# Kernel optimization log

Hardware: AMD Instinct MI355X
Metric: run time of the kernel (lower is better)

The kernel has to match this reference:

```python
import jax, jax.numpy as jnp
import numpy as np

B, N, D = 1, 4096, 512
H, HD = 8, 64
NBINS = 512
CAND = 64
SCALE = 1.0 / np.sqrt(HD)
MAX_NORM = 1.0 - 1e-5
TWO_PI = 2.0 * np.pi


def _project(x):
    # Poincare-ball style projection: clip L2 norm of each point to MAX_NORM.
    n = jnp.sqrt(jnp.sum(x * x, axis=-1, keepdims=True))
    s = jnp.minimum(1.0, MAX_NORM / jnp.maximum(n, 1e-12))
    return x * s


def _bins(x):
    # Deterministic geometric binning (DavisCache stand-in): quantize the
    # angle of the first two coordinates into NBINS bins.
    ang = jnp.arctan2(x[..., 1], x[..., 0])  # (-pi, pi]
    b = jnp.floor((ang / TWO_PI + 0.5) * NBINS)
    return jnp.clip(b, 0, NBINS - 1).astype(jnp.int32)


def setup_inputs() -> dict:
    key0 = jax.random.key(0)
    ks = jax.random.split(key0, 12)
    w = 0.02  # typical init scale for projection weights
    return {
        "query": jax.random.normal(ks[0], (B, N, D), dtype=jnp.float32),
        "key": jax.random.normal(ks[1], (B, N, D), dtype=jnp.float32),
        "value": jax.random.normal(ks[2], (B, N, D), dtype=jnp.float32),
        "Wq": jax.random.normal(ks[3], (D, D), dtype=jnp.float32) * w,
        "bq": jnp.zeros((D,), dtype=jnp.float32),
        "Wk": jax.random.normal(ks[4], (D, D), dtype=jnp.float32) * w,
        "bk": jnp.zeros((D,), dtype=jnp.float32),
        "Wv": jax.random.normal(ks[5], (D, D), dtype=jnp.float32) * w,
        "bv": jnp.zeros((D,), dtype=jnp.float32),
        "Wo": jax.random.normal(ks[6], (D, D), dtype=jnp.float32) * w,
        "bo": jnp.zeros((D,), dtype=jnp.float32),
    }


def reference(query, key, value, Wq, bq, Wk, bk, Wv, bv, Wo, bo):
    Bq, Nq, Dm = query.shape
    Nk = key.shape[1]
    # projections + split heads -> (B, H, N, HD)
    q = (query @ Wq.T + bq).reshape(Bq, Nq, H, HD).transpose(0, 2, 1, 3)
    k = (key @ Wk.T + bk).reshape(Bq, Nk, H, HD).transpose(0, 2, 1, 3)
    v = (value @ Wv.T + bv).reshape(Bq, Nk, H, HD).transpose(0, 2, 1, 3)
    q = _project(q)
    k = _project(k)

    # geometric binning; candidate keys for a query are those whose bin is
    # within radius 1 of the query's bin (neighboring_bins, radius=1).
    qb = _bins(q)  # (B, H, Nq) int32
    kb = _bins(k)  # (B, H, Nk) int32
    mask = jnp.abs(qb[..., :, None] - kb[..., None, :]) <= 1  # (B,H,Nq,Nk)
    # fallback: if a query has no candidates, attend over all keys
    any_valid = jnp.any(mask, axis=-1, keepdims=True)
    eff = jnp.where(any_valid, mask, True)
    # keep only the first CAND candidates per query (by key index)
    rank = jnp.cumsum(eff.astype(jnp.int32), axis=-1) - 1
    sel = eff & (rank < CAND)

    scores = jnp.einsum("bhqd,bhkd->bhqk", q, k) * SCALE
    scores = jnp.where(sel, scores, -jnp.inf)
    attn = jax.nn.softmax(scores, axis=-1)  # dropout p=0.0 (eval mode)
    out = jnp.einsum("bhqk,bhkd->bhqd", attn, v)

    out = out.transpose(0, 2, 1, 3).reshape(Bq, Nq, Dm)
    return out @ Wo.T + bo
```

## Files before the change

kernel.cpp:

```cpp
#include <hip/hip_runtime.h>
#include <math.h>

typedef unsigned short u16;
typedef __attribute__((ext_vector_type(8))) short v8bf;
typedef __attribute__((ext_vector_type(4))) float f32x4;

#define N_TOK 4096
#define DMODEL 512
#define NHEAD 8
#define HDIM 64
#define CANDN 64
#define NBINS 512
#define BINCAP 64
#define QCAP 128
#define ATT_SCALE 0.125f
#define MAX_NORM_F 0.99999f

__device__ __forceinline__ float bf2f(u16 u) {
  union { unsigned int i; float f; } v; v.i = ((unsigned int)u) << 16; return v.f;
}
__device__ __forceinline__ u16 f2bf(float f) {
  union { float f; unsigned int i; } v; v.f = f;
  unsigned int x = v.i;
  return (u16)((x + 0x7fffu + ((x >> 16) & 1u)) >> 16);
}
__device__ __forceinline__ uint4 load_pack8(const float* __restrict__ p) {
  const float4 x0 = *(const float4*)p;
  const float4 x1 = *(const float4*)(p + 4);
  union { u16 h[8]; uint4 u; } r;
  r.h[0] = f2bf(x0.x); r.h[1] = f2bf(x0.y); r.h[2] = f2bf(x0.z); r.h[3] = f2bf(x0.w);
  r.h[4] = f2bf(x1.x); r.h[5] = f2bf(x1.y); r.h[6] = f2bf(x1.z); r.h[7] = f2bf(x1.w);
  return r.u;
}

__global__ __launch_bounds__(256) void prep_kernel(
    const float* __restrict__ query, const float* __restrict__ key_,
    const float* __restrict__ value,
    const float* __restrict__ Wq, const float* __restrict__ Wk,
    const float* __restrict__ Wv, const float* __restrict__ Wo,
    u16* __restrict__ qx, u16* __restrict__ kx, u16* __restrict__ vx,
    u16* __restrict__ wqx, u16* __restrict__ wkx, u16* __restrict__ wvx,
    u16* __restrict__ wox,
    int* __restrict__ qb, int* __restrict__ kb, unsigned char* __restrict__ flags,
    int* __restrict__ khist)
{
  __shared__ float xs[16 * 516];
  const int blk = blockIdx.x;
  const int tid = threadIdx.x;

  if (blk >= 512) {
    const int base = ((blk - 512) << 8) + tid;
    for (int u = base; u < 919552; u += 262144) {
      if (u < 786432) {
        const int third = u >> 18;
        const int off = (u & 262143) << 3;
        const float* src = (third == 0) ? query : (third == 1) ? key_ : value;
        u16* dst = (third == 0) ? qx : (third == 1) ? kx : vx;
        *(uint4*)(dst + off) = load_pack8(src + off);
      } else if (u < 917504) {
        const int r2 = u - 786432;
        const int w = r2 >> 15;
        const int off = (r2 & 32767) << 3;
        const float* src = (w == 0) ? Wq : (w == 1) ? Wk : (w == 2) ? Wv : Wo;
        u16* dst = (w == 0) ? wqx : (w == 1) ? wkx : (w == 2) ? wvx : wox;
        *(uint4*)(dst + off) = load_pack8(src + off);
      } else {
        int4 z4; z4.x = 0; z4.y = 0; z4.z = 0; z4.w = 0;
        ((int4*)khist)[u - 917504] = z4;
      }
    }
    return;
  }

  const int isk  = blk >> 8;
  const int tile = blk & 255;
  const float* X = isk ? key_ : query;
  const float* W = isk ? Wk : Wq;

#pragma unroll
  for (int i = 0; i < 8; ++i) {
    const int flat = i * 1024 + tid * 4;
    const int row = flat >> 9, col = flat & 511;
    *(float4*)&xs[row * 516 + col] = *(const float4*)(X + (tile * 16 + row) * DMODEL + col);
  }
  __syncthreads();

  const int n_local = tid >> 4;
  const int pair = tid & 15;
  const int h = pair >> 1, coord = pair & 1;
  const float* wrow = W + ((h << 6) + coord) * DMODEL;
  const float* xrow = &xs[n_local * 516];

  double c0 = 0.0, c1 = 0.0, c2 = 0.0, c3 = 0.0;
  for (int k = 0; k < DMODEL; k += 4) {
    const float4 xv = *(const float4*)(xrow + k);
    const float4 wv = *(const float4*)(wrow + k);
    c0 = fma((double)xv.x, (double)wv.x, c0);
    c1 = fma((double)xv.y, (double)wv.y, c1);
    c2 = fma((double)xv.z, (double)wv.z, c2);
    c3 = fma((double)xv.w, (double)wv.w, c3);
  }
  const double a = (c0 + c1) + (c2 + c3);
  const double other = __shfl_xor(a, 1);
  if (coord == 0) {
    const double a0 = a, a1 = other;
    const int n = tile * 16 + n_local;
    double ang = atan2(a1, a0);
    double t = (ang / 6.283185307179586 + 0.5) * 512.0;
    int b = (int)floor(t);
    b = b < 0 ? 0 : (b > 511 ? 511 : b);
    (isk ? kb : qb)[(h << 12) + n] = b;

    const double r = sqrt(a0 * a0 + a1 * a1);
    const double dist = fabs(t - nearbyint(t));
    const double margin = fmin(0.45, 3.3e-4 / fmax(r, 1e-30) + 5e-5);
    flags[(isk << 15) | (h << 12) | n] = (dist < margin) ? 1 : 0;
  }
}

__device__ float fdlibm_atanf(float x) {
#pragma clang fp contract(off)
  const float atanhi[4] = {4.6364760399e-01f, 7.8539812565e-01f,
                           9.8279368877e-01f, 1.5707962513e+00f};
  const float atanlo[4] = {5.0121582440e-09f, 3.7748947079e-08f,
                           3.4473217170e-08f, 7.5497894159e-08f};
  const float aT[5] = {3.3333328366e-01f, -1.9999158382e-01f, 1.4253635705e-01f,
                       -1.0648017377e-01f, 6.1687607318e-02f};
  unsigned ix = __float_as_uint(x);
  const unsigned sign = ix >> 31;
  ix &= 0x7fffffffu;
  int id;
  float z, w, s1, s2;
  if (ix >= 0x4c800000u) {
    z = atanhi[3] + 0x1p-120f;
    return sign ? -z : z;
  }
  if (ix < 0x3ee00000u) {
    if (ix < 0x39800000u) return x;
    id = -1;
  } else {
    x = fabsf(x);
    if (ix < 0x3f980000u) {
      if (ix < 0x3f300000u) { id = 0; x = (2.0f * x - 1.0f) / (2.0f + x); }
      else                  { id = 1; x = (x - 1.0f) / (x + 1.0f); }
    } else {
      if (ix < 0x401c0000u) { id = 2; x = (x - 1.5f) / (1.0f + 1.5f * x); }
      else                  { id = 3; x = -1.0f / x; }
    }
  }
  z = x * x;
  w = z * z;
  s1 = z * (aT[0] + w * (aT[2] + w * aT[4]));
  s2 = w * (aT[1] + w * aT[3]);
  if (id < 0) return x - x * (s1 + s2);
  z = atanhi[id] - ((x * (s1 + s2) - atanlo[id]) - x);
  return sign ? -z : z;
}

__device__ float fdlibm_atan2f(float y, float x) {
#pragma clang fp contract(off)
  const float pi = 3.1415927410e+00f, pi_lo = -8.7422776573e-08f;
  const unsigned hx = __float_as_uint(x), hy = __float_as_uint(y);
  if (hx == 0x3f800000u) return fdlibm_atanf(y);
  const unsigned m = ((hy >> 31) & 1u) | ((hx >> 30) & 2u);
  const unsigned ix = hx & 0x7fffffffu, iy = hy & 0x7fffffffu;
  if (iy == 0u) {
    switch (m) { case 0: case 1: return y; case 2: return pi; default: return -pi; }
  }
  if (ix == 0u) return (m & 1u) ? -1.57079637050628662f : 1.57079637050628662f;
  float z;
  if (ix + (26u << 23) < iy) {
    z = 1.57079637050628662f;
    return (m & 1u) ? -z : z;
  }
  if ((m & 2u) && iy + (26u << 23) < ix) z = 0.0f;
  else z = fdlibm_atanf(fabsf(y / x));
  switch (m) {
    case 0: return z;
    case 1: return -z;
    case 2: return pi - (z - pi_lo);
    default: return (z - pi_lo) - pi;
  }
}

__global__ __launch_bounds__(256) void binfix_kernel(
    const float* __restrict__ query, const float* __restrict__ key_,
    const float* __restrict__ Wq, const float* __restrict__ Wk,
    const unsigned char* __restrict__ flags,
    int* __restrict__ qb, int* __restrict__ kb)
{
  __shared__ int wle[64];
  __shared__ int wlc;

  const int tid = threadIdx.x;
  const int slice = blockIdx.x;

  if (tid == 0) wlc = 0;
  __syncthreads();
  if (tid < 128) {
    const int flat = (slice << 7) + tid;
    if (flags[flat]) {
      const int p = atomicAdd(&wlc, 1);
      if (p < 64) wle[p] = flat;
    }
  }
  __syncthreads();
  int nw = wlc; if (nw > 64) nw = 64;
  const int w = tid >> 6, d = tid & 63;
  for (int e = w; e < nw; e += 4) {
    const int flat = wle[e];
    const int n = flat & 4095;
    const int h = (flat >> 12) & 7;
    const int isk = flat >> 15;
    const float* xr = (isk ? key_ : query) + n * DMODEL;
    const float* wr = (isk ? Wk : Wq) + ((h << 6) + d) * DMODEL;
    float acc = 0.0f;
    for (int k = 0; k < DMODEL; k += 16) {
      const float4 xa = *(const float4*)(xr + k);
      const float4 xb = *(const float4*)(xr + k + 4);
      const float4 xc = *(const float4*)(xr + k + 8);
      const float4 xd = *(const float4*)(xr + k + 12);
      const float4 wa = *(const float4*)(wr + k);
      const float4 wb = *(const float4*)(wr + k + 4);
      const float4 wc = *(const float4*)(wr + k + 8);
      const float4 wd = *(const float4*)(wr + k + 12);
      acc = __fmaf_rn(xa.x, wa.x, acc); acc = __fmaf_rn(xa.y, wa.y, acc);
      acc = __fmaf_rn(xa.z, wa.z, acc); acc = __fmaf_rn(xa.w, wa.w, acc);
      acc = __fmaf_rn(xb.x, wb.x, acc); acc = __fmaf_rn(xb.y, wb.y, acc);
      acc = __fmaf_rn(xb.z, wb.z, acc); acc = __fmaf_rn(xb.w, wb.w, acc);
      acc = __fmaf_rn(xc.x, wc.x, acc); acc = __fmaf_rn(xc.y, wc.y, acc);
      acc = __fmaf_rn(xc.z, wc.z, acc); acc = __fmaf_rn(xc.w, wc.w, acc);
      acc = __fmaf_rn(xd.x, wd.x, acc); acc = __fmaf_rn(xd.y, wd.y, acc);
      acc = __fmaf_rn(xd.z, wd.z, acc); acc = __fmaf_rn(xd.w, wd.w, acc);
    }
    {
#pragma clang fp contract(off)
      const float sq = acc * acc;
      float rr[8];
#pragma unroll
      for (int j = 0; j < 8; ++j) rr[j] = __shfl(sq, j);
      for (int i = 8; i < 64; i += 8) {
#pragma unroll
        for (int j = 0; j < 8; ++j) rr[j] += __shfl(sq, i + j);
      }
      const float ss = ((rr[0] + rr[1]) + (rr[2] + rr[3])) +
                       ((rr[4] + rr[5]) + (rr[6] + rr[7]));
      const float nrm = __fsqrt_rn(ss);
      const float s = fminf(1.0f, 0.99999f / fmaxf(nrm, 1e-12f));
      const float c0 = __shfl(acc, 0) * s;
      const float c1 = __shfl(acc, 1) * s;
      const float cr = (float)atan2((double)c1, (double)c0);
      const float fd = fdlibm_atan2f(c1, c0);
      const float tol = fmaxf(fabsf(cr) * 6e-7f, 1e-30f);
      const float ang = (fabsf(fd - cr) <= tol) ? fd : cr;
      const float t = ((ang / 6.2831854820251465f) + 0.5f) * 512.0f;
      int b = (int)floorf(t);
      b = b < 0 ? 0 : (b > 511 ? 511 : b);
      if (d == 0) (isk ? kb : qb)[(h << 12) + n] = b;
    }
  }
}

__global__ __launch_bounds__(256) void gemm_qkv_kernel(
    const u16* __restrict__ qx, const u16* __restrict__ kx, const u16* __restrict__ vx,
    const u16* __restrict__ wqx, const u16* __restrict__ wkx, const u16* __restrict__ wvx,
    const float* __restrict__ bq, const float* __restrict__ bk, const float* __restrict__ bv,
    u16* __restrict__ Qb, u16* __restrict__ Kb, u16* __restrict__ Vb)
{
  __shared__ u16 As[2][128 * 40];
  __shared__ u16 Ws[2][128 * 40];

  const int blk = blockIdx.x;
  const int tid = threadIdx.x;

  const int z = blk >> 7;
  const int rem = blk & 127;
  const int bm = (rem & 31) * 128;
  const int bn = (rem >> 5) * 128;

  const u16* A    = (z == 0) ? qx : (z == 1) ? kx : vx;
  const u16* W    = (z == 0) ? wqx : (z == 1) ? wkx : wvx;
  const float* bias = (z == 0) ? bq : (z == 1) ? bk : bv;
  u16* O          = (z == 0) ? Qb : (z == 1) ? Kb : Vb;

  const int lane = tid & 63;
  const int wave = tid >> 6;
  const int row4 = tid >> 2;
  const int seg  = tid & 3;
  const int wm = (wave & 1) * 64;
  const int wn = (wave >> 1) * 64;
  const int l15 = lane & 15;
  const int quad = lane >> 4;

  f32x4 acc[4][4] = {};

  uint4 a0 = *(const uint4*)(A + (bm + row4) * DMODEL + seg * 8);
  uint4 a1 = *(const uint4*)(A + (bm + row4 + 64) * DMODEL + seg * 8);
  uint4 w0 = *(const uint4*)(W + (bn + row4) * DMODEL + seg * 8);
  uint4 w1 = *(const uint4*)(W + (bn + row4 + 64) * DMODEL + seg * 8);

  for (int kt = 0; kt < DMODEL; kt += 32) {
    const int p = (kt >> 5) & 1;
    *(uint4*)&As[p][row4 * 40 + seg * 8] = a0;
    *(uint4*)&As[p][(row4 + 64) * 40 + seg * 8] = a1;
    *(uint4*)&Ws[p][row4 * 40 + seg * 8] = w0;
    *(uint4*)&Ws[p][(row4 + 64) * 40 + seg * 8] = w1;
    __syncthreads();
    if (kt + 32 < DMODEL) {
      a0 = *(const uint4*)(A + (bm + row4) * DMODEL + kt + 32 + seg * 8);
      a1 = *(const uint4*)(A + (bm + row4 + 64) * DMODEL + kt + 32 + seg * 8);
      w0 = *(const uint4*)(W + (bn + row4) * DMODEL + kt + 32 + seg * 8);
      w1 = *(const uint4*)(W + (bn + row4 + 64) * DMODEL + kt + 32 + seg * 8);
    }
    v8bf af[4], bfr[4];
#pragma unroll
    for (int i = 0; i < 4; ++i)
      af[i] = *(const v8bf*)&As[p][(wm + i * 16 + l15) * 40 + quad * 8];
#pragma unroll
    for (int j = 0; j < 4; ++j)
      bfr[j] = *(const v8bf*)&Ws[p][(wn + j * 16 + l15) * 40 + quad * 8];
#pragma unroll
    for (int i = 0; i < 4; ++i)
#pragma unroll
      for (int j = 0; j < 4; ++j)
        acc[i][j] = __builtin_amdgcn_mfma_f32_16x16x32_bf16(af[i], bfr[j], acc[i][j], 0, 0, 0);
  }

  float bval[4];
#pragma unroll
  for (int j = 0; j < 4; ++j) bval[j] = bias[bn + wn + j * 16 + l15];
  const int h = (bn + wn) >> 6;

#pragma unroll
  for (int i = 0; i < 4; ++i) {
#pragma unroll
    for (int r = 0; r < 4; ++r) {
      const int row = bm + wm + i * 16 + quad * 4 + r;
      float v0 = acc[i][0][r] + bval[0];
      float v1 = acc[i][1][r] + bval[1];
      float v2 = acc[i][2][r] + bval[2];
      float v3 = acc[i][3][r] + bval[3];
      if (z != 2) {
        float ss = v0 * v0 + v1 * v1 + v2 * v2 + v3 * v3;
#pragma unroll
        for (int o = 1; o < 16; o <<= 1) ss += __shfl_xor(ss, o);
        const float s = fminf(1.0f, MAX_NORM_F / fmaxf(sqrtf(ss), 1e-12f));
        v0 *= s; v1 *= s; v2 *= s; v3 *= s;
      }
      const int base = (((h << 12) + row) << 6) + l15;
      O[base +  0] = f2bf(v0); O[base + 16] = f2bf(v1);
      O[base + 32] = f2bf(v2); O[base + 48] = f2bf(v3);
    }
  }
}

__global__ __launch_bounds__(256) void bin_hist_kernel(
    const int* __restrict__ kb, const int* __restrict__ qb,
    int* __restrict__ khist, u16* __restrict__ blist,
    int* __restrict__ qhist, u16* __restrict__ qlist)
{
  const int h = blockIdx.x;
  const int type = blockIdx.y;
  const int* src = type ? qb : kb;
  int* hist = type ? qhist : khist;
  u16* list = type ? qlist : blist;
  const int cap = type ? QCAP : BINCAP;

  const int i = blockIdx.z * 256 + threadIdx.x;
  const int b = src[(h << 12) + i];
  const int pos = atomicAdd(&hist[(h << 9) + b], 1);
  if (pos < cap) list[((h << 9) + b) * cap + pos] = (u16)i;
}

__global__ __launch_bounds__(64) void attn_bin_kernel(
    const u16* __restrict__ Qb, const u16* __restrict__ Kb,
    const u16* __restrict__ Vb, const int* __restrict__ qhist,
    const u16* __restrict__ qlist, const int* __restrict__ khist,
    const u16* __restrict__ blist, u16* __restrict__ aout)
{
  __shared__ u16 kf[4 * 2 * 4 * 16 * 8];
  __shared__ u16 vf[4 * 2 * 4 * 16 * 8];
  __shared__ u16 pf[16 * 72];
  __shared__ u16 s_cand[64];
  __shared__ int s_qg[16];

  const int hb = blockIdx.x;
  const int h = hb >> 9;
  const int b = hb & 511;
  int qcnt = qhist[hb];
  if (qcnt > QCAP) qcnt = QCAP;
  if (qcnt == 0) return;

  const int lane = threadIdx.x;
  const int l15 = lane & 15;
  const int quad = lane >> 4;

  int v0 = 0xFFFF, v1 = 0xFFFF, v2 = 0xFFFF;
  int c0 = 0, c1 = 0, c2 = 0;
  if (b > 0) {
    c0 = khist[(h << 9) + b - 1];
    if (c0 > BINCAP) c0 = BINCAP;
    if (lane < c0) v0 = (int)blist[(((h << 9) + b - 1) << 6) + lane];
  }
  {
    c1 = khist[(h << 9) + b];
    if (c1 > BINCAP) c1 = BINCAP;
    if (lane < c1) v1 = (int)blist[(((h << 9) + b) << 6) + lane];
  }
  if (b < NBINS - 1) {
    c2 = khist[(h << 9) + b + 1];
    if (c2 > BINCAP) c2 = BINCAP;
    if (lane < c2) v2 = (int)blist[(((h << 9) + b + 1) << 6) + lane];
  }

  int r0 = 0, r1 = 0, r2 = 0;
#pragma unroll 8
  for (int j = 0; j < 64; ++j) {
    const int w0 = __shfl(v0, j);
    const int w1 = __shfl(v1, j);
    const int w2 = __shfl(v2, j);
    r0 += (w0 < v0) + (w1 < v0) + (w2 < v0);
    r1 += (w0 < v1) + (w1 < v1) + (w2 < v1);
    r2 += (w0 < v2) + (w1 < v2) + (w2 < v2);
  }
  const int tot = c0 + c1 + c2;
  const int ccnt = tot < CANDN ? tot : CANDN;
  const int ccnt_eff = (tot == 0) ? 64 : ccnt;
  if (tot == 0) {
    s_cand[lane] = (u16)lane;
  } else {
    if (v0 != 0xFFFF && r0 < CANDN) s_cand[r0] = (u16)v0;
    if (v1 != 0xFFFF && r1 < CANDN) s_cand[r1] = (u16)v1;
    if (v2 != 0xFFFF && r2 < CANDN) s_cand[r2] = (u16)v2;
  }
  __syncthreads();
  if (tot > 0 && lane >= ccnt) s_cand[lane] = s_cand[0];
  __syncthreads();

  {
    const int r = lane >> 3, s = lane & 7;
    const int ks = s >> 2, qd = s & 3;
#pragma unroll
    for (int it = 0; it < 8; ++it) {
      const int key = it * 8 + r;
      const int c = s_cand[key];
      const uint4 kv = *(const uint4*)(Kb + ((h << 18) | (c << 6)) + s * 8);
      const int idx = ((((key >> 4) * 2 + ks) * 4 + qd) * 16 + (key & 15)) * 8;
      *(uint4*)&kf[idx] = kv;
    }
  }
  {
    const int r = lane >> 3, s = lane & 7;
    const int nt = s >> 1, d0 = (s & 1) * 8;
#pragma unroll
    for (int it = 0; it < 8; ++it) {
      const int key = it * 8 + r;
      const int c = s_cand[key];
      union { u16 hh[8]; uint4 u; } vv;
      vv.u = *(const uint4*)(Vb + ((h << 18) | (c << 6)) + s * 8);
      const int kstep = key >> 5, qd = (key >> 3) & 3, j = key & 7;
#pragma unroll
      for (int m = 0; m < 8; ++m)
        vf[(((nt * 2 + kstep) * 4 + qd) * 16 + d0 + m) * 8 + j] = vv.hh[m];
    }
  }
  __syncthreads();

  v8bf akf[4][2], bvf[4][2];
#pragma unroll
  for (int t = 0; t < 4; ++t)
#pragma unroll
    for (int ks = 0; ks < 2; ++ks) {
      akf[t][ks] = *(const v8bf*)&kf[(((t * 2 + ks) * 4 + quad) * 16 + l15) * 8];
      bvf[t][ks] = *(const v8bf*)&vf[(((t * 2 + ks) * 4 + quad) * 16 + l15) * 8];
    }

  const int nchunk = (qcnt + 15) >> 4;
  for (int ci = 0; ci < nchunk; ++ci) {
    const int base = ci << 4;
    const int qcn = min(16, qcnt - base);
    __syncthreads();
    if (lane < 16) {
      int idx = base + lane;
      if (idx > qcnt - 1) idx = qcnt - 1;
      s_qg[lane] = (int)qlist[(hb << 7) + idx];
    }
    __syncthreads();

    const u16* qrow = Qb + ((h << 18) | (s_qg[l15] << 6));
    v8bf bq[2];
#pragma unroll
    for (int ks = 0; ks < 2; ++ks)
      bq[ks] = *(const v8bf*)(qrow + ks * 32 + quad * 8);

    float sc[16];
    __builtin_amdgcn_s_setprio(1);
#pragma unroll
    for (int t = 0; t < 4; ++t) {
      f32x4 sa = {0.f, 0.f, 0.f, 0.f};
      sa = __builtin_amdgcn_mfma_f32_16x16x32_bf16(akf[t][0], bq[0], sa, 0, 0, 0);
      sa = __builtin_amdgcn_mfma_f32_16x16x32_bf16(akf[t][1], bq[1], sa, 0, 0, 0);
#pragma unroll
      for (int r = 0; r < 4; ++r) {
        const int key = t * 16 + quad * 4 + r;
        sc[t * 4 + r] = (key < ccnt_eff) ? sa[r] * ATT_SCALE : -INFINITY;
      }
    }
    __builtin_amdgcn_s_setprio(0);
    float mx = sc[0];
#pragma unroll
    for (int i = 1; i < 16; ++i) mx = fmaxf(mx, sc[i]);
    mx = fmaxf(mx, __shfl_xor(mx, 16));
    mx = fmaxf(mx, __shfl_xor(mx, 32));
    float sum = 0.0f;
    float pe[16];
#pragma unroll
    for (int i = 0; i < 16; ++i) { pe[i] = __expf(sc[i] - mx); sum += pe[i]; }
    sum += __shfl_xor(sum, 16);
    sum += __shfl_xor(sum, 32);
    const float inv = 1.0f / sum;

    __syncthreads();
#pragma unroll
    for (int t = 0; t < 4; ++t)
#pragma unroll
      for (int r = 0; r < 4; ++r)
        pf[l15 * 72 + t * 16 + quad * 4 + r] = f2bf(pe[t * 4 + r] * inv);
    __syncthreads();

    v8bf ap[2];
#pragma unroll
    for (int ks = 0; ks < 2; ++ks)
      ap[ks] = *(const v8bf*)&pf[l15 * 72 + ks * 32 + quad * 8];

    __builtin_amdgcn_s_setprio(1);
#pragma unroll
    for (int nt = 0; nt < 4; ++nt) {
      f32x4 o = {0.f, 0.f, 0.f, 0.f};
      o = __builtin_amdgcn_mfma_f32_16x16x32_bf16(ap[0], bvf[nt][0], o, 0, 0, 0);
      o = __builtin_amdgcn_mfma_f32_16x16x32_bf16(ap[1], bvf[nt][1], o, 0, 0, 0);
#pragma unroll
      for (int r = 0; r < 4; ++r) {
        const int row = quad * 4 + r;
        if (row < qcn)
          aout[s_qg[row] * DMODEL + (h << 6) + nt * 16 + l15] = f2bf(o[r]);
      }
    }
    __builtin_amdgcn_s_setprio(0);
  }
}

__global__ __launch_bounds__(256) void gemm_out_kernel(
    const u16* __restrict__ A, const u16* __restrict__ W,
    const float* __restrict__ bias, float* __restrict__ O)
{
  __shared__ u16 As[2][64 * 40];
  __shared__ u16 Ws[2][128 * 40];

  const int tid  = threadIdx.x;
  const int lane = tid & 63;
  const int wave = tid >> 6;
  const int row4 = tid >> 2;
  const int seg  = tid & 3;

  const int bm = blockIdx.x * 64;
  const int bn = blockIdx.y * 128;
  const int wm = (wave & 1) * 32;
  const int wn = (wave >> 1) * 64;
  const int l15 = lane & 15;
  const int quad = lane >> 4;

  f32x4 acc[2][4] = {};

  uint4 a0 = *(const uint4*)(A + (bm + row4) * DMODEL + seg * 8);
  uint4 w0 = *(const uint4*)(W + (bn + row4) * DMODEL + seg * 8);
  uint4 w1 = *(const uint4*)(W + (bn + row4 + 64) * DMODEL + seg * 8);

  for (int kt = 0; kt < DMODEL; kt += 32) {
    const int p = (kt >> 5) & 1;
    *(uint4*)&As[p][row4 * 40 + seg * 8] = a0;
    *(uint4*)&Ws[p][row4 * 40 + seg * 8] = w0;
    *(uint4*)&Ws[p][(row4 + 64) * 40 + seg * 8] = w1;
    __syncthreads();
    if (kt + 32 < DMODEL) {
      a0 = *(const uint4*)(A + (bm + row4) * DMODEL + kt + 32 + seg * 8);
      w0 = *(const uint4*)(W + (bn + row4) * DMODEL + kt + 32 + seg * 8);
      w1 = *(const uint4*)(W + (bn + row4 + 64) * DMODEL + kt + 32 + seg * 8);
    }
    v8bf af[2], bfr[4];
#pragma unroll
    for (int i = 0; i < 2; ++i)
      af[i] = *(const v8bf*)&As[p][(wm + i * 16 + l15) * 40 + quad * 8];
#pragma unroll
    for (int j = 0; j < 4; ++j)
      bfr[j] = *(const v8bf*)&Ws[p][(wn + j * 16 + l15) * 40 + quad * 8];
#pragma unroll
    for (int i = 0; i < 2; ++i)
#pragma unroll
      for (int j = 0; j < 4; ++j)
        acc[i][j] = __builtin_amdgcn_mfma_f32_16x16x32_bf16(af[i], bfr[j], acc[i][j], 0, 0, 0);
  }

#pragma unroll
  for (int j = 0; j < 4; ++j) {
    const int cg = bn + wn + j * 16 + l15;
    const float bval = bias[cg];
#pragma unroll
    for (int i = 0; i < 2; ++i) {
      const int rbase = bm + wm + i * 16 + quad * 4;
#pragma unroll
      for (int r = 0; r < 4; ++r)
        O[(rbase + r) * DMODEL + cg] = acc[i][j][r] + bval;
    }
  }
}

extern "C" void kernel_launch(void* const* d_in, const int* in_sizes, int n_in,
                              void* d_out, int out_size, void* d_ws, size_t ws_size,
                              hipStream_t stream) {
  const float* query = (const float*)d_in[0];
  const float* key_  = (const float*)d_in[1];
  const float* value = (const float*)d_in[2];
  const float* Wq = (const float*)d_in[3];
  const float* bq = (const float*)d_in[4];
  const float* Wk = (const float*)d_in[5];
  const float* bk = (const float*)d_in[6];
  const float* Wv = (const float*)d_in[7];
  const float* bv = (const float*)d_in[8];
  const float* Wo = (const float*)d_in[9];
  const float* bo = (const float*)d_in[10];

  char* ws = (char*)d_ws;
  u16* qx    = (u16*)(ws);
  u16* kx    = (u16*)(ws + 4194304);
  u16* vx    = (u16*)(ws + 8388608);
  u16* wqx   = (u16*)(ws + 12582912);
  u16* wkx   = (u16*)(ws + 13107200);
  u16* wvx   = (u16*)(ws + 13631488);
  u16* wox   = (u16*)(ws + 14155776);
  u16* Qb    = (u16*)(ws + 14680064);
  u16* Kb    = (u16*)(ws + 18874368);
  u16* Vb    = (u16*)(ws + 23068672);
  u16* aout  = (u16*)(ws + 27262976);
  int* qb    = (int*)(ws + 31457280);
  int* kb    = (int*)(ws + 31588352);
  unsigned char* flags = (unsigned char*)(ws + 31719424);
  int* khist = (int*)(ws + 31784960);
  int* qhist = (int*)(ws + 31801344);
  u16* blist = (u16*)(ws + 31817728);
  u16* qlist = (u16*)(ws + 32342016);

  prep_kernel<<<1536, 256, 0, stream>>>(
      query, key_, value, Wq, Wk, Wv, Wo,
      qx, kx, vx, wqx, wkx, wvx, wox, qb, kb, flags, khist);
  binfix_kernel<<<512, 256, 0, stream>>>(
      query, key_, Wq, Wk, flags, qb, kb);
  gemm_qkv_kernel<<<384, 256, 0, stream>>>(
      qx, kx, vx, wqx, wkx, wvx, bq, bk, bv, Qb, Kb, Vb);
  bin_hist_kernel<<<dim3(8, 2, 16), 256, 0, stream>>>(
      kb, qb, khist, blist, qhist, qlist);
  attn_bin_kernel<<<4096, 64, 0, stream>>>(
      Qb, Kb, Vb, qhist, qlist, khist, blist, aout);
  gemm_out_kernel<<<dim3(64, 4), 256, 0, stream>>>(aout, wox, bo, (float*)d_out);
}
```

Measured before the change: 200.3 us.

## Fuse fp32-to-bf16 activation conversion into QKV GEMM and shrink GEMM tiles

The separate pass that converted query/key/value to bf16 in the prep kernel is removed. The QKV GEMM now reads fp32 activations directly and packs them to bf16 while staging into shared memory, which avoids writing and re-reading about 12 MB of intermediates. The QKV GEMM M-tile drops from 128 to 64 rows (768 blocks), and the output GEMM tile becomes 64x64 (512 blocks), giving more blocks for occupancy. The cost is twice the fp32 activation bytes per load inside the GEMM, redundant conversion of A across N-tiles, and less data reuse per block.

```diff
diff --git a/kernel.cpp b/kernel.cpp
--- a/kernel.cpp
+++ b/kernel.cpp
@@ -32,13 +32,17 @@
   r.h[4] = f2bf(x1.x); r.h[5] = f2bf(x1.y); r.h[6] = f2bf(x1.z); r.h[7] = f2bf(x1.w);
   return r.u;
 }
+__device__ __forceinline__ uint4 pack8v(const float4 x0, const float4 x1) {
+  union { u16 h[8]; uint4 u; } r;
+  r.h[0] = f2bf(x0.x); r.h[1] = f2bf(x0.y); r.h[2] = f2bf(x0.z); r.h[3] = f2bf(x0.w);
+  r.h[4] = f2bf(x1.x); r.h[5] = f2bf(x1.y); r.h[6] = f2bf(x1.z); r.h[7] = f2bf(x1.w);
+  return r.u;
+}
 
 __global__ __launch_bounds__(256) void prep_kernel(
     const float* __restrict__ query, const float* __restrict__ key_,
-    const float* __restrict__ value,
     const float* __restrict__ Wq, const float* __restrict__ Wk,
     const float* __restrict__ Wv, const float* __restrict__ Wo,
-    u16* __restrict__ qx, u16* __restrict__ kx, u16* __restrict__ vx,
     u16* __restrict__ wqx, u16* __restrict__ wkx, u16* __restrict__ wvx,
     u16* __restrict__ wox,
     int* __restrict__ qb, int* __restrict__ kb, unsigned char* __restrict__ flags,
@@ -49,25 +53,16 @@
   const int tid = threadIdx.x;
 
   if (blk >= 512) {
-    const int base = ((blk - 512) << 8) + tid;
-    for (int u = base; u < 919552; u += 262144) {
-      if (u < 786432) {
-        const int third = u >> 18;
-        const int off = (u & 262143) << 3;
-        const float* src = (third == 0) ? query : (third == 1) ? key_ : value;
-        u16* dst = (third == 0) ? qx : (third == 1) ? kx : vx;
-        *(uint4*)(dst + off) = load_pack8(src + off);
-      } else if (u < 917504) {
-        const int r2 = u - 786432;
-        const int w = r2 >> 15;
-        const int off = (r2 & 32767) << 3;
-        const float* src = (w == 0) ? Wq : (w == 1) ? Wk : (w == 2) ? Wv : Wo;
-        u16* dst = (w == 0) ? wqx : (w == 1) ? wkx : (w == 2) ? wvx : wox;
-        *(uint4*)(dst + off) = load_pack8(src + off);
-      } else {
-        int4 z4; z4.x = 0; z4.y = 0; z4.z = 0; z4.w = 0;
-        ((int4*)khist)[u - 917504] = z4;
-      }
+    const int u = ((blk - 512) << 8) + tid;
+    if (u < 131072) {
+      const int w = u >> 15;
+      const int off = (u & 32767) << 3;
+      const float* src = (w == 0) ? Wq : (w == 1) ? Wk : (w == 2) ? Wv : Wo;
+      u16* dst = (w == 0) ? wqx : (w == 1) ? wkx : (w == 2) ? wvx : wox;
+      *(uint4*)(dst + off) = load_pack8(src + off);
+    } else if (u < 133120) {
+      int4 z4; z4.x = 0; z4.y = 0; z4.z = 0; z4.w = 0;
+      ((int4*)khist)[u - 131072] = z4;
     }
     return;
   }
@@ -262,65 +257,65 @@
 }
 
 __global__ __launch_bounds__(256) void gemm_qkv_kernel(
-    const u16* __restrict__ qx, const u16* __restrict__ kx, const u16* __restrict__ vx,
+    const float* __restrict__ query, const float* __restrict__ key_,
+    const float* __restrict__ value,
     const u16* __restrict__ wqx, const u16* __restrict__ wkx, const u16* __restrict__ wvx,
     const float* __restrict__ bq, const float* __restrict__ bk, const float* __restrict__ bv,
     u16* __restrict__ Qb, u16* __restrict__ Kb, u16* __restrict__ Vb)
 {
-  __shared__ u16 As[2][128 * 40];
+  __shared__ u16 As[2][64 * 40];
   __shared__ u16 Ws[2][128 * 40];
 
   const int blk = blockIdx.x;
   const int tid = threadIdx.x;
 
-  const int z = blk >> 7;
-  const int rem = blk & 127;
-  const int bm = (rem & 31) * 128;
-  const int bn = (rem >> 5) * 128;
-
-  const u16* A    = (z == 0) ? qx : (z == 1) ? kx : vx;
+  const int z = blk >> 8;
+  const int rem = blk & 255;
+  const int bm = (rem & 63) * 64;
+  const int bn = (rem >> 6) * 128;
+
+  const float* X  = (z == 0) ? query : (z == 1) ? key_ : value;
   const u16* W    = (z == 0) ? wqx : (z == 1) ? wkx : wvx;
   const float* bias = (z == 0) ? bq : (z == 1) ? bk : bv;
   u16* O          = (z == 0) ? Qb : (z == 1) ? Kb : Vb;
 
   const int lane = tid & 63;
   const int wave = tid >> 6;
-  const int row4 = tid >> 2;
-  const int seg  = tid & 3;
-  const int wm = (wave & 1) * 64;
+  const int ra  = tid >> 2;
+  const int oa  = (tid & 3) * 8;
+  const int wm = (wave & 1) * 32;
   const int wn = (wave >> 1) * 64;
   const int l15 = lane & 15;
   const int quad = lane >> 4;
 
-  f32x4 acc[4][4] = {};
-
-  uint4 a0 = *(const uint4*)(A + (bm + row4) * DMODEL + seg * 8);
-  uint4 a1 = *(const uint4*)(A + (bm + row4 + 64) * DMODEL + seg * 8);
-  uint4 w0 = *(const uint4*)(W + (bn + row4) * DMODEL + seg * 8);
-  uint4 w1 = *(const uint4*)(W + (bn + row4 + 64) * DMODEL + seg * 8);
+  f32x4 acc[2][4] = {};
+
+  float4 a0f = *(const float4*)(X + (bm + ra) * DMODEL + oa);
+  float4 a1f = *(const float4*)(X + (bm + ra) * DMODEL + oa + 4);
+  uint4 w0 = *(const uint4*)(W + (bn + ra) * DMODEL + oa);
+  uint4 w1 = *(const uint4*)(W + (bn + ra + 64) * DMODEL + oa);
 
   for (int kt = 0; kt < DMODEL; kt += 32) {
     const int p = (kt >> 5) & 1;
-    *(uint4*)&As[p][row4 * 40 + seg * 8] = a0;
-    *(uint4*)&As[p][(row4 + 64) * 40 + seg * 8] = a1;
-    *(uint4*)&Ws[p][row4 * 40 + seg * 8] = w0;
-    *(uint4*)&Ws[p][(row4 + 64) * 40 + seg * 8] = w1;
+    *(uint4*)&As[p][ra * 40 + oa] = pack8v(a0f, a1f);
+    *(uint4*)&Ws[p][ra * 40 + oa] = w0;
+    *(uint4*)&Ws[p][(ra + 64) * 40 + oa] = w1;
     __syncthreads();
     if (kt + 32 < DMODEL) {
-      a0 = *(const uint4*)(A + (bm + row4) * DMODEL + kt + 32 + seg * 8);
-      a1 = *(const uint4*)(A + (bm + row4 + 64) * DMODEL + kt + 32 + seg * 8);
-      w0 = *(const uint4*)(W + (bn + row4) * DMODEL + kt + 32 + seg * 8);
-      w1 = *(const uint4*)(W + (bn + row4 + 64) * DMODEL + kt + 32 + seg * 8);
-    }
-    v8bf af[4], bfr[4];
-#pragma unroll
-    for (int i = 0; i < 4; ++i)
+      a0f = *(const float4*)(X + (bm + ra) * DMODEL + kt + 32 + oa);
+      a1f = *(const float4*)(X + (bm + ra) * DMODEL + kt + 32 + oa + 4);
+      w0 = *(const uint4*)(W + (bn + ra) * DMODEL + kt + 32 + oa);
+      w1 = *(const uint4*)(W + (bn + ra + 64) * DMODEL + kt + 32 + oa);
+    }
+    v8bf af[2], bfr[4];
+#pragma unroll
+    for (int i = 0; i < 2; ++i)
       af[i] = *(const v8bf*)&As[p][(wm + i * 16 + l15) * 40 + quad * 8];
 #pragma unroll
     for (int j = 0; j < 4; ++j)
       bfr[j] = *(const v8bf*)&Ws[p][(wn + j * 16 + l15) * 40 + quad * 8];
 #pragma unroll
-    for (int i = 0; i < 4; ++i)
+    for (int i = 0; i < 2; ++i)
 #pragma unroll
       for (int j = 0; j < 4; ++j)
         acc[i][j] = __builtin_amdgcn_mfma_f32_16x16x32_bf16(af[i], bfr[j], acc[i][j], 0, 0, 0);
@@ -332,7 +327,7 @@
   const int h = (bn + wn) >> 6;
 
 #pragma unroll
-  for (int i = 0; i < 4; ++i) {
+  for (int i = 0; i < 2; ++i) {
 #pragma unroll
     for (int r = 0; r < 4; ++r) {
       const int row = bm + wm + i * 16 + quad * 4 + r;
@@ -555,54 +550,51 @@
     const float* __restrict__ bias, float* __restrict__ O)
 {
   __shared__ u16 As[2][64 * 40];
-  __shared__ u16 Ws[2][128 * 40];
+  __shared__ u16 Ws[2][64 * 40];
 
   const int tid  = threadIdx.x;
   const int lane = tid & 63;
   const int wave = tid >> 6;
-  const int row4 = tid >> 2;
-  const int seg  = tid & 3;
+  const int ra  = tid >> 2;
+  const int oa  = (tid & 3) * 8;
 
   const int bm = blockIdx.x * 64;
-  const int bn = blockIdx.y * 128;
+  const int bn = blockIdx.y * 64;
   const int wm = (wave & 1) * 32;
-  const int wn = (wave >> 1) * 64;
+  const int wn = (wave >> 1) * 32;
   const int l15 = lane & 15;
   const int quad = lane >> 4;
 
-  f32x4 acc[2][4] = {};
-
-  uint4 a0 = *(const uint4*)(A + (bm + row4) * DMODEL + seg * 8);
-  uint4 w0 = *(const uint4*)(W + (bn + row4) * DMODEL + seg * 8);
-  uint4 w1 = *(const uint4*)(W + (bn + row4 + 64) * DMODEL + seg * 8);
+  f32x4 acc[2][2] = {};
+
+  uint4 a0 = *(const uint4*)(A + (bm + ra) * DMODEL + oa);
+  uint4 w0 = *(const uint4*)(W + (bn + ra) * DMODEL + oa);
 
   for (int kt = 0; kt < DMODEL; kt += 32) {
     const int p = (kt >> 5) & 1;
-    *(uint4*)&As[p][row4 * 40 + seg * 8] = a0;
-    *(uint4*)&Ws[p][row4 * 40 + seg * 8] = w0;
-    *(uint4*)&Ws[p][(row4 + 64) * 40 + seg * 8] = w1;
+    *(uint4*)&As[p][ra * 40 + oa] = a0;
+    *(uint4*)&Ws[p][ra * 40 + oa] = w0;
     __syncthreads();
     if (kt + 32 < DMODEL) {
-      a0 = *(const uint4*)(A + (bm + row4) * DMODEL + kt + 32 + seg * 8);
-      w0 = *(const uint4*)(W + (bn + row4) * DMODEL + kt + 32 + seg * 8);
-      w1 = *(const uint4*)(W + (bn + row4 + 64) * DMODEL + kt + 32 + seg * 8);
-    }
-    v8bf af[2], bfr[4];
+      a0 = *(const uint4*)(A + (bm + ra) * DMODEL + kt + 32 + oa);
+      w0 = *(const uint4*)(W + (bn + ra) * DMODEL + kt + 32 + oa);
+    }
+    v8bf af[2], bfr[2];
 #pragma unroll
     for (int i = 0; i < 2; ++i)
       af[i] = *(const v8bf*)&As[p][(wm + i * 16 + l15) * 40 + quad * 8];
 #pragma unroll
-    for (int j = 0; j < 4; ++j)
+    for (int j = 0; j < 2; ++j)
       bfr[j] = *(const v8bf*)&Ws[p][(wn + j * 16 + l15) * 40 + quad * 8];
 #pragma unroll
     for (int i = 0; i < 2; ++i)
 #pragma unroll
-      for (int j = 0; j < 4; ++j)
+      for (int j = 0; j < 2; ++j)
         acc[i][j] = __builtin_amdgcn_mfma_f32_16x16x32_bf16(af[i], bfr[j], acc[i][j], 0, 0, 0);
   }
 
 #pragma unroll
-  for (int j = 0; j < 4; ++j) {
+  for (int j = 0; j < 2; ++j) {
     const int cg = bn + wn + j * 16 + l15;
     const float bval = bias[cg];
 #pragma unroll
@@ -631,9 +623,6 @@
   const float* bo = (const float*)d_in[10];
 
   char* ws = (char*)d_ws;
-  u16* qx    = (u16*)(ws);
-  u16* kx    = (u16*)(ws + 4194304);
-  u16* vx    = (u16*)(ws + 8388608);
   u16* wqx   = (u16*)(ws + 12582912);
   u16* wkx   = (u16*)(ws + 13107200);
   u16* wvx   = (u16*)(ws + 13631488);
@@ -650,16 +639,16 @@
   u16* blist = (u16*)(ws + 31817728);
   u16* qlist = (u16*)(ws + 32342016);
 
-  prep_kernel<<<1536, 256, 0, stream>>>(
-      query, key_, value, Wq, Wk, Wv, Wo,
-      qx, kx, vx, wqx, wkx, wvx, wox, qb, kb, flags, khist);
+  prep_kernel<<<1032, 256, 0, stream>>>(
+      query, key_, Wq, Wk, Wv, Wo,
+      wqx, wkx, wvx, wox, qb, kb, flags, khist);
   binfix_kernel<<<512, 256, 0, stream>>>(
       query, key_, Wq, Wk, flags, qb, kb);
-  gemm_qkv_kernel<<<384, 256, 0, stream>>>(
-      qx, kx, vx, wqx, wkx, wvx, bq, bk, bv, Qb, Kb, Vb);
+  gemm_qkv_kernel<<<768, 256, 0, stream>>>(
+      query, key_, value, wqx, wkx, wvx, bq, bk, bv, Qb, Kb, Vb);
   bin_hist_kernel<<<dim3(8, 2, 16), 256, 0, stream>>>(
       kb, qb, khist, blist, qhist, qlist);
   attn_bin_kernel<<<4096, 64, 0, stream>>>(
       Qb, Kb, Vb, qhist, qlist, khist, blist, aout);
-  gemm_out_kernel<<<dim3(64, 4), 256, 0, stream>>>(aout, wox, bo, (float*)d_out);
-}
+  gemm_out_kernel<<<dim3(64, 8), 256, 0, stream>>>(aout, wox, bo, (float*)d_out);
+}
```

Result: no change. 200.3 us (-0.0%).
